# Kernel optimization log

Measured on AMD Instinct MI355X. Metric: run time of the kernel, lower is better.

Reference implementation:

```python
import jax, jax.numpy as jnp
import numpy as np

B, T, C, H = 4, 2048, 1024, 16
D = C // H

def setup_inputs() -> dict:
    key = jax.random.key(0)
    k1, k2, k3, k4 = jax.random.split(key, 4)
    s = 1.0 / np.sqrt(C)
    return {
        "x": jax.random.normal(k1, (B, T, C), dtype=jnp.float32),
        "W_qkv": jax.random.normal(k2, (3 * C, C), dtype=jnp.float32) * s,
        "W_out": jax.random.normal(k3, (C, C), dtype=jnp.float32) * s,
        "b_out": jax.random.normal(k4, (C,), dtype=jnp.float32) * s,
    }

def reference(x, W_qkv, W_out, b_out):
    Bx, Tx, Cx = x.shape
    # qkv projection (torch Linear: y = x @ W.T), bias=False
    qkv = x @ W_qkv.T                               # [B,T,3C]
    q, k, v = jnp.split(qkv, 3, axis=-1)
    def heads(t):
        return t.reshape(Bx, Tx, H, D).transpose(0, 2, 1, 3)  # [B,H,T,D]
    q, k, v = heads(q), heads(k), heads(v)
    scale = 1.0 / jnp.sqrt(jnp.asarray(D, dtype=x.dtype))
    scores = jnp.einsum("bhqd,bhkd->bhqk", q, k) * scale      # [B,H,T,T]
    causal = jnp.tril(jnp.ones((Tx, Tx), dtype=bool))
    scores = jnp.where(causal[None, None], scores, -jnp.inf)
    attn = jax.nn.softmax(scores, axis=-1)                    # dropout p=0 (eval)
    out = jnp.einsum("bhqk,bhkd->bhqd", attn, v)              # [B,H,T,D]
    out = out.transpose(0, 2, 1, 3).reshape(Bx, Tx, Cx)       # [B,T,C]
    return out @ W_out.T + b_out
```

## Files before the change

kernel.cpp:

```cpp
#include <hip/hip_runtime.h>


typedef __attribute__((ext_vector_type(8))) __bf16 bf16x8;
typedef __attribute__((ext_vector_type(4))) float f32x4;
typedef __attribute__((ext_vector_type(16))) float f32x16;

__device__ __forceinline__ unsigned short f2bf(float f) {
  union { float f; unsigned u; } v; v.f = f;
  unsigned r = v.u + 0x7fffu + ((v.u >> 16) & 1u);
  return (unsigned short)(r >> 16);
}

__device__ __forceinline__ unsigned cvtpk(float lo, float hi) {
  unsigned r;
  asm("v_cvt_pk_bf16_f32 %0, %1, %2" : "=v"(r) : "v"(lo), "v"(hi));
  return r;
}

__device__ __forceinline__ float fexp2(float x) {
  float r;
  asm("v_exp_f32 %0, %1" : "=v"(r) : "v"(x));
  return r;
}
__device__ __forceinline__ float max3f(float a, float b, float c) {
  return fmaxf(fmaxf(a, b), c);
}

__device__ __forceinline__ void gld16(const void* g, void* l) {
  __builtin_amdgcn_global_load_lds(
      (const __attribute__((address_space(1))) void*)g,
      (__attribute__((address_space(3))) void*)l, 16, 0, 0);
}

__device__ __forceinline__ f32x4 mfma16(bf16x8 a, bf16x8 b, f32x4 c) {
  return __builtin_amdgcn_mfma_f32_16x16x32_bf16(a, b, c, 0, 0, 0);
}
__device__ __forceinline__ f32x16 mfma32(bf16x8 a, bf16x8 b, f32x16 c) {
  return __builtin_amdgcn_mfma_f32_32x32x16_bf16(a, b, c, 0, 0, 0);
}

__global__ __launch_bounds__(256) void cast_all(
    const float* __restrict__ x, const float* __restrict__ wq,
    const float* __restrict__ wo, unsigned short* __restrict__ xb,
    unsigned short* __restrict__ wqb, unsigned short* __restrict__ wob) {
  int i = (blockIdx.x * 256 + threadIdx.x) * 4;
  const float* s;
  unsigned short* d;
  int off;
  if (i < 8388608) { s = x; d = xb; off = i; }
  else if (i < 11534336) { s = wq; d = wqb; off = i - 8388608; }
  else { s = wo; d = wob; off = i - 11534336; }
  float4 v = *(const float4*)(s + off);
  ushort4 o;
  o.x = f2bf(v.x); o.y = f2bf(v.y); o.z = f2bf(v.z); o.w = f2bf(v.w);
  *(ushort4*)(d + off) = o;
}

__device__ __forceinline__ bf16x8 ldsw128(const char* mat, int row, int cb) {
  return *(const bf16x8*)(mat + row * 128 + (cb ^ ((row & 7) << 4)));
}

#define PH_SYNC_A() do { __builtin_amdgcn_s_barrier();              \
    asm volatile("s_waitcnt lgkmcnt(0)" ::: "memory");              \
    __builtin_amdgcn_sched_barrier(0); } while (0)
#define PH_SYNC_B() do { __builtin_amdgcn_s_barrier();              \
    __builtin_amdgcn_sched_barrier(0); } while (0)
#define VMC6() asm volatile("s_waitcnt vmcnt(6)" ::: "memory")
#define VMC2() asm volatile("s_waitcnt vmcnt(2)" ::: "memory")
#define VMC0() asm volatile("s_waitcnt vmcnt(0)" ::: "memory")

__device__ __forceinline__ void stage_half(const char* gbase, char* mat,
                                           int kt, int half, int tid) {
#pragma unroll
  for (int q = 0; q < 2; ++q) {
    const int r = half * 128 + q * 64 + (tid >> 3);
    const int cb = (tid & 7) * 16;
    gld16(gbase + (size_t)r * 2048 + kt * 128 + (cb ^ ((r & 7) << 4)),
          mat + r * 128 + cb);
  }
}
__device__ __forceinline__ void stage_A(const char* gbase, char* mat,
                                        int kt, int tid) {
#pragma unroll
  for (int q = 0; q < 2; ++q) {
    const int r = q * 64 + (tid >> 3);
    const int cb = (tid & 7) * 16;
    gld16(gbase + (size_t)r * 2048 + kt * 128 + (cb ^ ((r & 7) << 4)),
          mat + r * 128 + cb);
  }
}

template <int MODE>
__global__ __launch_bounds__(512, 2) void gemm2p(
    const unsigned short* __restrict__ A, const unsigned short* __restrict__ Bm,
    unsigned short* __restrict__ qo, unsigned short* __restrict__ ko,
    unsigned short* __restrict__ vo,
    const float* __restrict__ bias, float* __restrict__ fout) {
  __shared__ char lds[98304];
  const int tid = threadIdx.x;
  const int w = tid >> 6, l = tid & 63, lr = l & 15, lg = l >> 4;
  const int wm = w >> 2, wn = w & 3;
  constexpr int GX = (MODE == 0) ? 12 : 4;
  constexpr int NWG = GX * 64;
  const int L = blockIdx.x + blockIdx.y * GX;
  const int logical = (L & 7) * (NWG >> 3) + (L >> 3);
  const int m0 = (logical / GX) * 128, n0 = (logical % GX) * 256;
  const char* Ag = (const char*)A + (size_t)m0 * 2048;
  const char* Bg = (const char*)Bm + (size_t)n0 * 2048;
  char* A0 = lds;            char* A1 = lds + 16384;
  char* B0 = lds + 32768;    char* B1 = lds + 65536;

  f32x4 acc[4][4];
  f32x4 zero = {0.f, 0.f, 0.f, 0.f};
#pragma unroll
  for (int i = 0; i < 4; i++)
#pragma unroll
    for (int jj = 0; jj < 4; jj++) acc[i][jj] = zero;

  stage_A(Ag, A0, 0, tid);
  stage_half(Bg, B0, 0, 0, tid);
  stage_half(Bg, B0, 0, 1, tid);
  stage_A(Ag, A1, 1, tid);
  stage_half(Bg, B1, 1, 0, tid);
  stage_half(Bg, B1, 1, 1, tid);
  VMC6();
  __builtin_amdgcn_s_barrier();
  __builtin_amdgcn_sched_barrier(0);

  for (int t = 0; t < 16; ++t) {
    char* As = (t & 1) ? A1 : A0;
    char* Bs = (t & 1) ? B1 : B0;
    char* Bo = (t & 1) ? B0 : B1;
    bf16x8 aF[4][2], bF[2][2];

#pragma unroll
    for (int mq = 0; mq < 4; ++mq) {
      const int row = (mq >> 1) * 64 + wm * 32 + (mq & 1) * 16 + lr;
#pragma unroll
      for (int kk = 0; kk < 2; ++kk)
        aF[mq][kk] = ldsw128(As, row, kk * 64 + lg * 16);
    }
#pragma unroll
    for (int nt = 0; nt < 2; ++nt) {
      const int row = wn * 64 + nt * 16 + lr;
#pragma unroll
      for (int kk = 0; kk < 2; ++kk)
        bF[nt][kk] = ldsw128(Bs, row, kk * 64 + lg * 16);
    }
    if (t >= 1 && t < 15) {
      stage_half(Bg, Bo, t + 1, 0, tid);
      stage_half(Bg, Bo, t + 1, 1, tid);
    }
    PH_SYNC_A();
    __builtin_amdgcn_s_setprio(1);
#pragma unroll
    for (int mq = 0; mq < 4; ++mq)
#pragma unroll
      for (int nt = 0; nt < 2; ++nt)
#pragma unroll
        for (int kk = 0; kk < 2; ++kk)
          acc[mq][nt] = mfma16(aF[mq][kk], bF[nt][kk], acc[mq][nt]);
    __builtin_amdgcn_s_setprio(0);
    PH_SYNC_B();

#pragma unroll
    for (int nt = 0; nt < 2; ++nt) {
      const int row = wn * 64 + (2 + nt) * 16 + lr;
#pragma unroll
      for (int kk = 0; kk < 2; ++kk)
        bF[nt][kk] = ldsw128(Bs, row, kk * 64 + lg * 16);
    }
    if (t < 14) stage_A(Ag, As, t + 2, tid);
    PH_SYNC_A();
    __builtin_amdgcn_s_setprio(1);
#pragma unroll
    for (int mq = 0; mq < 4; ++mq)
#pragma unroll
      for (int nt = 0; nt < 2; ++nt)
#pragma unroll
        for (int kk = 0; kk < 2; ++kk)
          acc[mq][2 + nt] = mfma16(aF[mq][kk], bF[nt][kk], acc[mq][2 + nt]);
    __builtin_amdgcn_s_setprio(0);
    if (t < 14) VMC2(); else if (t < 15) VMC0();
    PH_SYNC_B();
  }

  if (MODE == 1) {
#pragma unroll
    for (int mq = 0; mq < 4; ++mq) {
#pragma unroll
      for (int nt = 0; nt < 4; ++nt) {
        int n = n0 + wn * 64 + nt * 16 + lr;
        int mb = m0 + (mq >> 1) * 64 + wm * 32 + (mq & 1) * 16 + lg * 4;
        float bv = bias[n];
#pragma unroll
        for (int i = 0; i < 4; i++)
          fout[(size_t)(mb + i) * 1024 + n] = acc[mq][nt][i] + bv;
      }
    }
    return;
  }

  const int ty = n0 >> 10;
  const int hbase = (n0 & 1023) >> 6;
  const int bb = m0 >> 11;
  const int tloc = m0 & 2047;

  if (ty < 2) {
    unsigned short* dst = (ty == 0) ? qo : ko;
    const float sc = (ty == 0) ? 0.18033688011111687f : 1.0f;
    const int h = hbase + wn;
#pragma unroll
    for (int mq = 0; mq < 4; ++mq) {
#pragma unroll
      for (int nt = 0; nt < 4; ++nt) {
        const int dd = nt * 16 + lr;
        const int trow = tloc + (mq >> 1) * 64 + wm * 32 + (mq & 1) * 16 + lg * 4;
#pragma unroll
        for (int i = 0; i < 4; i++)
          dst[((size_t)(bb * 16 + h) * 2048 + trow + i) * 64 + dd] =
              f2bf(acc[mq][nt][i] * sc);
      }
    }
  } else {
#pragma unroll
    for (int mq = 0; mq < 4; ++mq) {
      const int mcb = ((mq >> 1) * 64 + wm * 32 + (mq & 1) * 16 + lg * 4) * 2;
#pragma unroll
      for (int nt = 0; nt < 4; ++nt) {
        const int row = wn * 64 + nt * 16 + lr;
        uint2 pk;
        pk.x = cvtpk(acc[mq][nt][0], acc[mq][nt][1]);
        pk.y = cvtpk(acc[mq][nt][2], acc[mq][nt][3]);
        *(uint2*)(lds + row * 256 + (mcb ^ ((row & 15) << 4))) = pk;
      }
    }
    __builtin_amdgcn_s_barrier();
    const int hi = tid >> 7, r = tid & 127;
    const int dd = r & 63, seg = r >> 6;
    const int nrow = hi * 64 + dd;
    unsigned short* gp = vo +
        ((size_t)(bb * 16 + hbase + hi) * 64 + dd) * 2048 + tloc + seg * 64;
#pragma unroll
    for (int j = 0; j < 8; ++j) {
      uint4 vd = *(const uint4*)(lds + nrow * 256 +
                                 ((seg * 128 + j * 16) ^ ((nrow & 15) << 4)));
      *(uint4*)(gp + j * 8) = vd;
    }
  }
}

__device__ __forceinline__ bf16x8 ldsw(const char* base, int row, int cb) {
  return *(const bf16x8*)(base + row * 128 + (cb ^ ((row & 7) << 4)));
}

__global__ __launch_bounds__(512, 4) void attn_causal(
    const unsigned short* __restrict__ qg, const unsigned short* __restrict__ kg,
    const unsigned short* __restrict__ vtg, unsigned short* __restrict__ og) {
  __shared__ char lds[32768];
  const int tid = threadIdx.x;
  const int w = tid >> 6, l = tid & 63, lo = l & 31, hi = l >> 5;
  const int bh = blockIdx.x;
  const int qc = (0x31204657u >> (blockIdx.y * 4)) & 7;
  const int q0 = qc * 256;
  const int nkv = qc * 4 + 4;
  const int b = bh >> 4, h = bh & 15;
  const char* kpB = (const char*)(kg + (size_t)bh * 131072);
  const char* vpB = (const char*)(vtg + (size_t)bh * 131072);
  const unsigned short* qp = qg + (size_t)bh * 131072;
  const int qrow = q0 + 8 * lo + w;

  bf16x8 qf[4];
#pragma unroll
  for (int c = 0; c < 4; ++c)
    qf[c] = *(const bf16x8*)(qp + (size_t)qrow * 64 + hi * 8 + c * 16);

  f32x16 ov[2];
#pragma unroll
  for (int r = 0; r < 16; ++r) { ov[0][r] = 0.f; ov[1][r] = 0.f; }
  const f32x16 zz = {0.f, 0.f, 0.f, 0.f, 0.f, 0.f, 0.f, 0.f,
                     0.f, 0.f, 0.f, 0.f, 0.f, 0.f, 0.f, 0.f};
  float m = -__builtin_inff(), lsum = 0.f;

  const int srow = tid >> 3;
  const int scb = ((tid & 7) * 16) ^ ((srow & 7) << 4);

  gld16(kpB + (size_t)srow * 128 + scb, lds + tid * 16);
  gld16(vpB + (size_t)srow * 4096 + scb, lds + 8192 + tid * 16);
  __syncthreads();

  for (int kt = 0; kt < nkv; ++kt) {
    const int k0 = kt * 64;
    if (kt + 1 < nkv) {
      char* nb = lds + ((kt + 1) & 1) * 16384;
      gld16(kpB + (size_t)(k0 + 64 + srow) * 128 + scb, nb + tid * 16);
      gld16(vpB + (size_t)srow * 4096 + (size_t)(k0 + 64) * 2 + scb, nb + 8192 + tid * 16);
    }
    const char* Kbuf = lds + (kt & 1) * 16384;
    const char* Vbuf = Kbuf + 8192;

    f32x16 sv[2];
    __builtin_amdgcn_s_setprio(1);
#pragma unroll
    for (int c = 0; c < 4; ++c) {
      bf16x8 kf0 = ldsw(Kbuf, lo, hi * 16 + c * 32);
      bf16x8 kf1 = ldsw(Kbuf, 32 + lo, hi * 16 + c * 32);
      if (c == 0) {
        sv[0] = mfma32(kf0, qf[0], zz);
        sv[1] = mfma32(kf1, qf[0], zz);
      } else {
        sv[0] = mfma32(kf0, qf[c], sv[0]);
        sv[1] = mfma32(kf1, qf[c], sv[1]);
      }
    }
    __builtin_amdgcn_s_setprio(0);

    if (kt >= nkv - 4) {
#pragma unroll
      for (int t = 0; t < 2; ++t)
#pragma unroll
        for (int r = 0; r < 16; ++r) {
          int kgl = k0 + t * 32 + (r & 3) + 8 * (r >> 2) + 4 * hi;
          if (kgl > qrow) sv[t][r] = -__builtin_inff();
        }
    }

    float t0m = max3f(sv[0][0], sv[0][1], sv[0][2]);
    float t1m = max3f(sv[0][3], sv[0][4], sv[0][5]);
    float t2m = max3f(sv[0][6], sv[0][7], sv[0][8]);
    float t3m = max3f(sv[0][9], sv[0][10], sv[0][11]);
    float t4m = max3f(sv[0][12], sv[0][13], sv[0][14]);
    float t5m = max3f(sv[0][15], sv[1][0], sv[1][1]);
    float t6m = max3f(sv[1][2], sv[1][3], sv[1][4]);
    float t7m = max3f(sv[1][5], sv[1][6], sv[1][7]);
    float t8m = max3f(sv[1][8], sv[1][9], sv[1][10]);
    float t9m = max3f(sv[1][11], sv[1][12], sv[1][13]);
    float tam = fmaxf(sv[1][14], sv[1][15]);
    float u0 = max3f(t0m, t1m, t2m);
    float u1 = max3f(t3m, t4m, t5m);
    float u2 = max3f(t6m, t7m, t8m);
    float u3 = fmaxf(t9m, tam);
    float tm = fmaxf(max3f(u0, u1, u2), u3);
    tm = fmaxf(tm, __shfl_xor(tm, 32, 64));

    if (!__all(tm <= m + 8.f)) {
      float nm = fmaxf(fmaxf(m, tm), -1e30f);
      float f = fexp2(m - nm);
      m = nm;
      lsum *= f;
#pragma unroll
      for (int r = 0; r < 16; ++r) { ov[0][r] *= f; ov[1][r] *= f; }
    }

    float ps0 = 0.f, ps1 = 0.f, ps2 = 0.f, ps3 = 0.f;
#pragma unroll
    for (int t = 0; t < 2; ++t)
#pragma unroll
      for (int r = 0; r < 16; r += 4) {
        float p0 = fexp2(sv[t][r + 0] - m);
        float p1 = fexp2(sv[t][r + 1] - m);
        float p2 = fexp2(sv[t][r + 2] - m);
        float p3 = fexp2(sv[t][r + 3] - m);
        sv[t][r + 0] = p0; sv[t][r + 1] = p1;
        sv[t][r + 2] = p2; sv[t][r + 3] = p3;
        ps0 += p0; ps1 += p1; ps2 += p2; ps3 += p3;
      }
    lsum += (ps0 + ps1) + (ps2 + ps3);

    __builtin_amdgcn_s_setprio(1);
#pragma unroll
    for (int c = 0; c < 4; ++c) {
      const int t = c >> 1, rb = (c & 1) * 8;
      unsigned wA = cvtpk(sv[t][rb + 0], sv[t][rb + 1]);
      unsigned wB = cvtpk(sv[t][rb + 2], sv[t][rb + 3]);
      unsigned wC = cvtpk(sv[t][rb + 4], sv[t][rb + 5]);
      unsigned wD = cvtpk(sv[t][rb + 6], sv[t][rb + 7]);
      asm volatile("v_permlane32_swap_b32 %0, %1" : "+v"(wA), "+v"(wC));
      asm volatile("v_permlane32_swap_b32 %0, %1" : "+v"(wB), "+v"(wD));
      union { uint4 u; bf16x8 h; } pc;
      pc.u.x = wA; pc.u.y = wB; pc.u.z = wC; pc.u.w = wD;
      bf16x8 vf0 = ldsw(Vbuf, lo, hi * 16 + c * 32);
      bf16x8 vf1 = ldsw(Vbuf, 32 + lo, hi * 16 + c * 32);
      ov[0] = mfma32(vf0, pc.h, ov[0]);
      ov[1] = mfma32(vf1, pc.h, ov[1]);
    }
    __builtin_amdgcn_s_setprio(0);
    __syncthreads();
  }

  float lt = lsum + __shfl_xor(lsum, 32, 64);
  float inv = 1.0f / lt;
  char* outl = lds + w * 4096;
#pragma unroll
  for (int t2 = 0; t2 < 2; ++t2)
#pragma unroll
    for (int rp = 0; rp < 8; ++rp) {
      const int r = rp * 2;
      const int d0 = (r & 3) + 8 * (r >> 2) + 4 * hi + 32 * t2;
      unsigned pw = cvtpk(ov[t2][r] * inv, ov[t2][r + 1] * inv);
      *(unsigned*)(outl + lo * 128 + ((d0 * 2) ^ ((lo & 7) << 4))) = pw;
    }
  __syncthreads();
  {
    const int qi = l >> 1, cbb = (l & 1) * 64;
    const int t = q0 + 8 * qi + w;
    unsigned short* gp = og + ((size_t)(b * 2048 + t)) * 1024 + h * 64 + (cbb >> 1);
#pragma unroll
    for (int i = 0; i < 4; ++i) {
      uint4 vdat = *(const uint4*)(outl + qi * 128 + ((cbb + i * 16) ^ ((qi & 7) << 4)));
      *(uint4*)(gp + i * 8) = vdat;
    }
  }
}

extern "C" void kernel_launch(void* const* d_in, const int* in_sizes, int n_in,
                              void* d_out, int out_size, void* d_ws, size_t ws_size,
                              hipStream_t stream) {
  const float* x = (const float*)d_in[0];
  const float* Wqkv = (const float*)d_in[1];
  const float* Wout = (const float*)d_in[2];
  const float* bout = (const float*)d_in[3];
  float* out = (float*)d_out;
  char* ws = (char*)d_ws;

  unsigned short* xb = (unsigned short*)(ws);
  unsigned short* wqb = (unsigned short*)(ws + 16777216);
  unsigned short* wob = (unsigned short*)(ws + 23068672);
  unsigned short* qb = (unsigned short*)(ws + 25165824);
  unsigned short* kb = (unsigned short*)(ws + 41943040);
  unsigned short* vtb = (unsigned short*)(ws + 58720256);
  unsigned short* ogb = xb;

  cast_all<<<12288, 256, 0, stream>>>(x, Wqkv, Wout, xb, wqb, wob);

  gemm2p<0><<<dim3(12, 64), 512, 0, stream>>>(xb, wqb, qb, kb, vtb, nullptr, nullptr);
  attn_causal<<<dim3(64, 8), 512, 0, stream>>>(qb, kb, vtb, ogb);
  gemm2p<1><<<dim3(4, 64), 512, 0, stream>>>(ogb, wob, nullptr, nullptr, nullptr, bout, out);
}
```

Measured before the change: 154.7 us.

## Stage K/V tiles in pairs of 128 keys to halve attention barriers

The causal attention loop now loads two 64-key K and V^T tiles per stage into a 64KB double-buffered LDS region and processes both before a single __syncthreads. It also uses a wider 256-byte swizzled V row layout. The goal is fewer barriers per key and larger async global loads in flight to hide latency. In exchange, launch bounds drop from 4 to 2 blocks per CU because of the doubled LDS, which lowers occupancy.

```diff
diff --git a/kernel.cpp b/kernel.cpp
--- a/kernel.cpp
+++ b/kernel.cpp
@@ -253,17 +253,21 @@
 __device__ __forceinline__ bf16x8 ldsw(const char* base, int row, int cb) {
   return *(const bf16x8*)(base + row * 128 + (cb ^ ((row & 7) << 4)));
 }
-
-__global__ __launch_bounds__(512, 4) void attn_causal(
+__device__ __forceinline__ bf16x8 ldswV(const char* base, int row, int cb) {
+  return *(const bf16x8*)(base + row * 256 + (cb ^ ((row & 15) << 4)));
+}
+
+__global__ __launch_bounds__(512, 2) void attn_causal(
     const unsigned short* __restrict__ qg, const unsigned short* __restrict__ kg,
     const unsigned short* __restrict__ vtg, unsigned short* __restrict__ og) {
-  __shared__ char lds[32768];
+  __shared__ char lds[65536];
   const int tid = threadIdx.x;
   const int w = tid >> 6, l = tid & 63, lo = l & 31, hi = l >> 5;
   const int bh = blockIdx.x;
   const int qc = (0x31204657u >> (blockIdx.y * 4)) & 7;
   const int q0 = qc * 256;
   const int nkv = qc * 4 + 4;
+  const int npair = nkv >> 1;
   const int b = bh >> 4, h = bh & 15;
   const char* kpB = (const char*)(kg + (size_t)bh * 131072);
   const char* vpB = (const char*)(vtg + (size_t)bh * 131072);
@@ -282,109 +286,122 @@
                      0.f, 0.f, 0.f, 0.f, 0.f, 0.f, 0.f, 0.f};
   float m = -__builtin_inff(), lsum = 0.f;
 
-  const int srow = tid >> 3;
-  const int scb = ((tid & 7) * 16) ^ ((srow & 7) << 4);
-
-  gld16(kpB + (size_t)srow * 128 + scb, lds + tid * 16);
-  gld16(vpB + (size_t)srow * 4096 + scb, lds + 8192 + tid * 16);
+  const int ksr = tid >> 3, kcb = (tid & 7) * 16;
+  const int vsr = tid >> 4, vcb = (tid & 15) * 16;
+
+#define STAGE_PAIR(p, buf) do {                                             \
+    char* kb_ = (buf);                                                      \
+    char* vb_ = (buf) + 16384;                                              \
+    _Pragma("unroll") for (int j = 0; j < 2; ++j) {                         \
+      const int kr = j * 64 + ksr;                                          \
+      gld16(kpB + (size_t)((p) * 128 + kr) * 128 + (kcb ^ ((kr & 7) << 4)), \
+            kb_ + j * 8192 + tid * 16);                                     \
+      const int vr = j * 32 + vsr;                                          \
+      gld16(vpB + (size_t)vr * 4096 + (p) * 256 + (vcb ^ ((vr & 15) << 4)), \
+            vb_ + j * 8192 + tid * 16);                                     \
+    }                                                                       \
+  } while (0)
+
+  STAGE_PAIR(0, lds);
   __syncthreads();
 
-  for (int kt = 0; kt < nkv; ++kt) {
-    const int k0 = kt * 64;
-    if (kt + 1 < nkv) {
-      char* nb = lds + ((kt + 1) & 1) * 16384;
-      gld16(kpB + (size_t)(k0 + 64 + srow) * 128 + scb, nb + tid * 16);
-      gld16(vpB + (size_t)srow * 4096 + (size_t)(k0 + 64) * 2 + scb, nb + 8192 + tid * 16);
-    }
-    const char* Kbuf = lds + (kt & 1) * 16384;
-    const char* Vbuf = Kbuf + 8192;
-
-    f32x16 sv[2];
-    __builtin_amdgcn_s_setprio(1);
-#pragma unroll
-    for (int c = 0; c < 4; ++c) {
-      bf16x8 kf0 = ldsw(Kbuf, lo, hi * 16 + c * 32);
-      bf16x8 kf1 = ldsw(Kbuf, 32 + lo, hi * 16 + c * 32);
-      if (c == 0) {
-        sv[0] = mfma32(kf0, qf[0], zz);
-        sv[1] = mfma32(kf1, qf[0], zz);
-      } else {
-        sv[0] = mfma32(kf0, qf[c], sv[0]);
-        sv[1] = mfma32(kf1, qf[c], sv[1]);
-      }
-    }
-    __builtin_amdgcn_s_setprio(0);
-
-    if (kt >= nkv - 4) {
+  for (int p = 0; p < npair; ++p) {
+    if (p + 1 < npair) STAGE_PAIR(p + 1, lds + ((p + 1) & 1) * 32768);
+    const char* Kbuf = lds + (p & 1) * 32768;
+    const char* Vbuf = Kbuf + 16384;
+
+#pragma unroll
+    for (int hh = 0; hh < 2; ++hh) {
+      const int kt = 2 * p + hh;
+      const int k0 = kt * 64;
+
+      f32x16 sv[2];
+      __builtin_amdgcn_s_setprio(1);
+#pragma unroll
+      for (int c = 0; c < 4; ++c) {
+        bf16x8 kf0 = ldsw(Kbuf, hh * 64 + lo, hi * 16 + c * 32);
+        bf16x8 kf1 = ldsw(Kbuf, hh * 64 + 32 + lo, hi * 16 + c * 32);
+        if (c == 0) {
+          sv[0] = mfma32(kf0, qf[0], zz);
+          sv[1] = mfma32(kf1, qf[0], zz);
+        } else {
+          sv[0] = mfma32(kf0, qf[c], sv[0]);
+          sv[1] = mfma32(kf1, qf[c], sv[1]);
+        }
+      }
+      __builtin_amdgcn_s_setprio(0);
+
+      if (kt >= nkv - 4) {
+#pragma unroll
+        for (int t = 0; t < 2; ++t)
+#pragma unroll
+          for (int r = 0; r < 16; ++r) {
+            int kgl = k0 + t * 32 + (r & 3) + 8 * (r >> 2) + 4 * hi;
+            if (kgl > qrow) sv[t][r] = -__builtin_inff();
+          }
+      }
+
+      float t0m = max3f(sv[0][0], sv[0][1], sv[0][2]);
+      float t1m = max3f(sv[0][3], sv[0][4], sv[0][5]);
+      float t2m = max3f(sv[0][6], sv[0][7], sv[0][8]);
+      float t3m = max3f(sv[0][9], sv[0][10], sv[0][11]);
+      float t4m = max3f(sv[0][12], sv[0][13], sv[0][14]);
+      float t5m = max3f(sv[0][15], sv[1][0], sv[1][1]);
+      float t6m = max3f(sv[1][2], sv[1][3], sv[1][4]);
+      float t7m = max3f(sv[1][5], sv[1][6], sv[1][7]);
+      float t8m = max3f(sv[1][8], sv[1][9], sv[1][10]);
+      float t9m = max3f(sv[1][11], sv[1][12], sv[1][13]);
+      float tam = fmaxf(sv[1][14], sv[1][15]);
+      float u0 = max3f(t0m, t1m, t2m);
+      float u1 = max3f(t3m, t4m, t5m);
+      float u2 = max3f(t6m, t7m, t8m);
+      float u3 = fmaxf(t9m, tam);
+      float tm = fmaxf(max3f(u0, u1, u2), u3);
+      tm = fmaxf(tm, __shfl_xor(tm, 32, 64));
+
+      if (!__all(tm <= m + 8.f)) {
+        float nm = fmaxf(fmaxf(m, tm), -1e30f);
+        float f = fexp2(m - nm);
+        m = nm;
+        lsum *= f;
+#pragma unroll
+        for (int r = 0; r < 16; ++r) { ov[0][r] *= f; ov[1][r] *= f; }
+      }
+
+      float ps0 = 0.f, ps1 = 0.f, ps2 = 0.f, ps3 = 0.f;
 #pragma unroll
       for (int t = 0; t < 2; ++t)
 #pragma unroll
-        for (int r = 0; r < 16; ++r) {
-          int kgl = k0 + t * 32 + (r & 3) + 8 * (r >> 2) + 4 * hi;
-          if (kgl > qrow) sv[t][r] = -__builtin_inff();
+        for (int r = 0; r < 16; r += 4) {
+          float p0 = fexp2(sv[t][r + 0] - m);
+          float p1 = fexp2(sv[t][r + 1] - m);
+          float p2 = fexp2(sv[t][r + 2] - m);
+          float p3 = fexp2(sv[t][r + 3] - m);
+          sv[t][r + 0] = p0; sv[t][r + 1] = p1;
+          sv[t][r + 2] = p2; sv[t][r + 3] = p3;
+          ps0 += p0; ps1 += p1; ps2 += p2; ps3 += p3;
         }
-    }
-
-    float t0m = max3f(sv[0][0], sv[0][1], sv[0][2]);
-    float t1m = max3f(sv[0][3], sv[0][4], sv[0][5]);
-    float t2m = max3f(sv[0][6], sv[0][7], sv[0][8]);
-    float t3m = max3f(sv[0][9], sv[0][10], sv[0][11]);
-    float t4m = max3f(sv[0][12], sv[0][13], sv[0][14]);
-    float t5m = max3f(sv[0][15], sv[1][0], sv[1][1]);
-    float t6m = max3f(sv[1][2], sv[1][3], sv[1][4]);
-    float t7m = max3f(sv[1][5], sv[1][6], sv[1][7]);
-    float t8m = max3f(sv[1][8], sv[1][9], sv[1][10]);
-    float t9m = max3f(sv[1][11], sv[1][12], sv[1][13]);
-    float tam = fmaxf(sv[1][14], sv[1][15]);
-    float u0 = max3f(t0m, t1m, t2m);
-    float u1 = max3f(t3m, t4m, t5m);
-    float u2 = max3f(t6m, t7m, t8m);
-    float u3 = fmaxf(t9m, tam);
-    float tm = fmaxf(max3f(u0, u1, u2), u3);
-    tm = fmaxf(tm, __shfl_xor(tm, 32, 64));
-
-    if (!__all(tm <= m + 8.f)) {
-      float nm = fmaxf(fmaxf(m, tm), -1e30f);
-      float f = fexp2(m - nm);
-      m = nm;
-      lsum *= f;
-#pragma unroll
-      for (int r = 0; r < 16; ++r) { ov[0][r] *= f; ov[1][r] *= f; }
-    }
-
-    float ps0 = 0.f, ps1 = 0.f, ps2 = 0.f, ps3 = 0.f;
-#pragma unroll
-    for (int t = 0; t < 2; ++t)
-#pragma unroll
-      for (int r = 0; r < 16; r += 4) {
-        float p0 = fexp2(sv[t][r + 0] - m);
-        float p1 = fexp2(sv[t][r + 1] - m);
-        float p2 = fexp2(sv[t][r + 2] - m);
-        float p3 = fexp2(sv[t][r + 3] - m);
-        sv[t][r + 0] = p0; sv[t][r + 1] = p1;
-        sv[t][r + 2] = p2; sv[t][r + 3] = p3;
-        ps0 += p0; ps1 += p1; ps2 += p2; ps3 += p3;
-      }
-    lsum += (ps0 + ps1) + (ps2 + ps3);
-
-    __builtin_amdgcn_s_setprio(1);
-#pragma unroll
-    for (int c = 0; c < 4; ++c) {
-      const int t = c >> 1, rb = (c & 1) * 8;
-      unsigned wA = cvtpk(sv[t][rb + 0], sv[t][rb + 1]);
-      unsigned wB = cvtpk(sv[t][rb + 2], sv[t][rb + 3]);
-      unsigned wC = cvtpk(sv[t][rb + 4], sv[t][rb + 5]);
-      unsigned wD = cvtpk(sv[t][rb + 6], sv[t][rb + 7]);
-      asm volatile("v_permlane32_swap_b32 %0, %1" : "+v"(wA), "+v"(wC));
-      asm volatile("v_permlane32_swap_b32 %0, %1" : "+v"(wB), "+v"(wD));
-      union { uint4 u; bf16x8 h; } pc;
-      pc.u.x = wA; pc.u.y = wB; pc.u.z = wC; pc.u.w = wD;
-      bf16x8 vf0 = ldsw(Vbuf, lo, hi * 16 + c * 32);
-      bf16x8 vf1 = ldsw(Vbuf, 32 + lo, hi * 16 + c * 32);
-      ov[0] = mfma32(vf0, pc.h, ov[0]);
-      ov[1] = mfma32(vf1, pc.h, ov[1]);
-    }
-    __builtin_amdgcn_s_setprio(0);
+      lsum += (ps0 + ps1) + (ps2 + ps3);
+
+      __builtin_amdgcn_s_setprio(1);
+#pragma unroll
+      for (int c = 0; c < 4; ++c) {
+        const int t = c >> 1, rb = (c & 1) * 8;
+        unsigned wA = cvtpk(sv[t][rb + 0], sv[t][rb + 1]);
+        unsigned wB = cvtpk(sv[t][rb + 2], sv[t][rb + 3]);
+        unsigned wC = cvtpk(sv[t][rb + 4], sv[t][rb + 5]);
+        unsigned wD = cvtpk(sv[t][rb + 6], sv[t][rb + 7]);
+        asm volatile("v_permlane32_swap_b32 %0, %1" : "+v"(wA), "+v"(wC));
+        asm volatile("v_permlane32_swap_b32 %0, %1" : "+v"(wB), "+v"(wD));
+        union { uint4 u; bf16x8 h; } pc;
+        pc.u.x = wA; pc.u.y = wB; pc.u.z = wC; pc.u.w = wD;
+        bf16x8 vf0 = ldswV(Vbuf, lo, hh * 128 + hi * 16 + c * 32);
+        bf16x8 vf1 = ldswV(Vbuf, 32 + lo, hh * 128 + hi * 16 + c * 32);
+        ov[0] = mfma32(vf0, pc.h, ov[0]);
+        ov[1] = mfma32(vf1, pc.h, ov[1]);
+      }
+      __builtin_amdgcn_s_setprio(0);
+    }
     __syncthreads();
   }
 
```

Measured after the change: 163.7 us. +5.8%, slower.
